# Kernel optimization log

Measured on AMD Instinct MI355X. Metric: run time of the kernel, lower is better.

The kernel has to match this reference:

```python
import jax, jax.numpy as jnp
import numpy as np

GROUP_SIZE = 128


def dequant_rtn(qweight, scale, zero_point):
    # qweight: [O, I] int, scale/zero_point: [O, I//GROUP_SIZE]
    O, I = qweight.shape
    G = scale.shape[1]
    gs = I // G
    q = qweight.reshape(O, G, gs).astype(jnp.float32)
    zp = zero_point.astype(jnp.float32)[:, :, None]
    w = (q - zp) * scale[:, :, None]
    return w.reshape(O, I)


def setup_inputs() -> dict:
    key = jax.random.key(0)
    k1, k2, k3, k4, k5 = jax.random.split(key, 5)
    B, S, I, O = 2, 2048, 4096, 11008
    G = I // GROUP_SIZE
    x = jax.random.normal(k1, (B, S, I), dtype=jnp.float32)
    qweight = jax.random.randint(k2, (O, I), 0, 16, dtype=jnp.int32)
    scale = jax.random.uniform(k3, (O, G), dtype=jnp.float32) * 0.02 + 1e-3
    zero_point = jax.random.randint(k4, (O, G), 0, 16, dtype=jnp.int32)
    bias = jax.random.normal(k5, (O,), dtype=jnp.float32)
    return {"x": x, "qweight": qweight, "scale": scale,
            "zero_point": zero_point, "bias": bias}


def reference(x, qweight, scale, zero_point, bias):
    # weight-only path: dequant weight, then F.linear(x, w, bias)
    w = dequant_rtn(qweight, scale, zero_point)  # [O, I] fp32
    return jnp.einsum('bsi,oi->bso', x, w) + bias
```

## Files before the change

### kernel.cpp

```cpp
#include <hip/hip_runtime.h>
#include <cstdint>
#include <cstddef>

typedef __attribute__((ext_vector_type(4))) int i32x4;
typedef __bf16 bf16;
typedef __attribute__((ext_vector_type(8))) __bf16 bf16x8;
typedef __attribute__((ext_vector_type(4))) float f32x4;

#define BM 128
#define BN 128
#define BKB 128
#define GROUP_M 16

__device__ __forceinline__ unsigned bf16_rne(float f) {
  unsigned u = __float_as_uint(f);
  unsigned r = 0x7FFFu + ((u >> 16) & 1u);
  return ((u + r) >> 16) & 0xFFFFu;
}
__device__ __forceinline__ unsigned pack2(float a, float b) {
  return bf16_rne(a) | (bf16_rne(b) << 16);
}
__device__ __forceinline__ int pack4i8(int a, int b, int c, int d) {
  return (a & 0xFF) | ((b & 0xFF) << 8) | ((c & 0xFF) << 16) | (d << 24);
}
__device__ __forceinline__ int q_i8(float v) {
  v = fminf(fmaxf(v, -127.0f), 127.0f);
  return __float2int_rn(v);
}

__global__ __launch_bounds__(256) void prep_kernel(
    const float* __restrict__ x, char* __restrict__ xq, float* __restrict__ xscale,
    int M,
    const int* __restrict__ q, const float* __restrict__ scale,
    const int* __restrict__ zp, char* __restrict__ wq, float* __restrict__ wscale,
    int K, int G) {
  __shared__ float red[4];
  const int b = blockIdx.x;
  const int tid = threadIdx.x;
  float f[16];

  if (b < M) {
    const float4* src = (const float4*)(x + (size_t)b * K);
#pragma unroll
    for (int i = 0; i < 4; ++i) {
      float4 v = src[tid + 256 * i];
      f[4 * i + 0] = v.x; f[4 * i + 1] = v.y;
      f[4 * i + 2] = v.z; f[4 * i + 3] = v.w;
    }
  } else {
    const int row = b - M;
    const int4* src = (const int4*)(q + (size_t)row * K);
    const float* srow = scale + (size_t)row * G;
    const int*   zrow = zp + (size_t)row * G;
#pragma unroll
    for (int i = 0; i < 4; ++i) {
      const int j = tid + 256 * i;
      const int g = j >> 5;
      const float s = srow[g];
      const float nzs = -s * (float)zrow[g];
      int4 qv = src[j];
      f[4 * i + 0] = fmaf((float)qv.x, s, nzs);
      f[4 * i + 1] = fmaf((float)qv.y, s, nzs);
      f[4 * i + 2] = fmaf((float)qv.z, s, nzs);
      f[4 * i + 3] = fmaf((float)qv.w, s, nzs);
    }
  }

  float m = 0.f;
#pragma unroll
  for (int j = 0; j < 16; ++j) m = fmaxf(m, fabsf(f[j]));
#pragma unroll
  for (int off = 32; off >= 1; off >>= 1) m = fmaxf(m, __shfl_xor(m, off));
  if ((tid & 63) == 0) red[tid >> 6] = m;
  __syncthreads();
  m = fmaxf(fmaxf(red[0], red[1]), fmaxf(red[2], red[3]));

  const float inv = m > 0.f ? 127.0f / m : 0.f;
  int pk[4];
#pragma unroll
  for (int i = 0; i < 4; ++i)
    pk[i] = pack4i8(q_i8(f[4 * i + 0] * inv), q_i8(f[4 * i + 1] * inv),
                    q_i8(f[4 * i + 2] * inv), q_i8(f[4 * i + 3] * inv));

  char* dst = (b < M) ? (xq + (size_t)b * K) : (wq + (size_t)(b - M) * K);
  int* dst_i32 = (int*)dst;
#pragma unroll
  for (int i = 0; i < 4; ++i) dst_i32[tid + 256 * i] = pk[i];

  if (tid == 0) {
    if (b < M) xscale[b] = m * (1.0f / 127.0f);
    else       wscale[b - M] = m * (1.0f / 127.0f);
  }
}

typedef __attribute__((address_space(1))) void gas_void;
typedef __attribute__((address_space(3))) void las_void;

__device__ __forceinline__ void load_lds16(const void* g, void* l) {
  __builtin_amdgcn_global_load_lds((gas_void*)g, (las_void*)l, 16, 0, 0);
}

__global__ __launch_bounds__(256) void gemm_i8_kernel(
    const char* __restrict__ A,
    const char* __restrict__ Bw,
    const float* __restrict__ ascale,
    const float* __restrict__ bscale,
    const float* __restrict__ bias,
    float* __restrict__ C,
    int M, int N, int K) {
  __shared__ __align__(16) char Alds[BM * BKB];
  __shared__ __align__(16) char Blds[BN * BKB];
  const int tid  = threadIdx.x;
  const int wave = tid >> 6;
  const int lane = tid & 63;
  const int quad = lane >> 4;
  const int l16  = lane & 15;

  const int nbm = M / BM;
  const int nbn = N / BN;
  int flat = blockIdx.x;
  int per_group = GROUP_M * nbn;
  int gid = flat / per_group;
  int rem = flat - gid * per_group;
  int gm = nbm - gid * GROUP_M;
  if (gm > GROUP_M) gm = GROUP_M;
  const int bm = (gid * GROUP_M + (rem % gm)) * BM;
  const int bn = (rem / gm) * BN;

  const int wm = (wave & 1) * 64;
  const int wn = (wave >> 1) * 64;

  i32x4 acc[4][4];
#pragma unroll
  for (int i = 0; i < 4; ++i)
#pragma unroll
    for (int j = 0; j < 4; ++j)
      acc[i][j] = (i32x4){0, 0, 0, 0};

  for (int kt = 0; kt < K; kt += BKB) {
#pragma unroll
    for (int t = 0; t < 4; ++t) {
      int s0 = (wave * 4 + t) * 64;
      int s  = s0 + lane;
      int m  = s >> 3;
      int kq = (s & 7) ^ (m & 7);
      load_lds16(A  + (size_t)(bm + m) * K + kt + kq * 16, &Alds[s0 * 16]);
      load_lds16(Bw + (size_t)(bn + m) * K + kt + kq * 16, &Blds[s0 * 16]);
    }
    __syncthreads();

#pragma unroll
    for (int ks = 0; ks < 2; ++ks) {
      i32x4 af[4], bfr[4];
#pragma unroll
      for (int tm = 0; tm < 4; ++tm) {
        int m  = wm + tm * 16 + l16;
        int kq = ks * 4 + quad;
        af[tm] = *(const i32x4*)&Alds[(m * 8 + (kq ^ (m & 7))) * 16];
      }
#pragma unroll
      for (int tn = 0; tn < 4; ++tn) {
        int n  = wn + tn * 16 + l16;
        int kq = ks * 4 + quad;
        bfr[tn] = *(const i32x4*)&Blds[(n * 8 + (kq ^ (n & 7))) * 16];
      }
#pragma unroll
      for (int tm = 0; tm < 4; ++tm)
#pragma unroll
        for (int tn = 0; tn < 4; ++tn)
          acc[tm][tn] = __builtin_amdgcn_mfma_i32_16x16x64_i8(
              af[tm], bfr[tn], acc[tm][tn], 0, 0, 0);
    }
    __syncthreads();
  }

#pragma unroll
  for (int tn = 0; tn < 4; ++tn) {
    int col = bn + wn + tn * 16 + l16;
    float bv = bias[col];
    float ws = bscale[col];
#pragma unroll
    for (int tm = 0; tm < 4; ++tm) {
      int row0 = bm + wm + tm * 16 + quad * 4;
#pragma unroll
      for (int v = 0; v < 4; ++v) {
        float val = ascale[row0 + v] * ws * (float)acc[tm][tn][v] + bv;
        __builtin_nontemporal_store(val, &C[(size_t)(row0 + v) * N + col]);
      }
    }
  }
}

__global__ __launch_bounds__(256) void gemm_fused_kernel(
    const float* __restrict__ X, const int* __restrict__ Q,
    const float* __restrict__ scale, const int* __restrict__ zp,
    const float* __restrict__ bias, float* __restrict__ C,
    int M, int N, int K, int G) {
  __shared__ __align__(16) bf16 Alds[128 * 64];
  __shared__ __align__(16) bf16 Blds[128 * 64];
  const int tid  = threadIdx.x;
  const int wave = tid >> 6;
  const int lane = tid & 63;
  const int quad = lane >> 4;
  const int l16  = lane & 15;
  const int bm = blockIdx.y * 128;
  const int bn = blockIdx.x * 128;
  const int wm = (wave & 1) * 64;
  const int wn = (wave >> 1) * 64;

  f32x4 acc[4][4];
#pragma unroll
  for (int i = 0; i < 4; ++i)
#pragma unroll
    for (int j = 0; j < 4; ++j)
      acc[i][j] = (f32x4){0.f, 0.f, 0.f, 0.f};

  for (int kt = 0; kt < K; kt += 64) {
#pragma unroll
    for (int i = 0; i < 4; ++i) {
      int c = tid + i * 256;
      int m = c >> 3;
      int kq = (c & 7) ^ (m & 7);
      const float* src = X + (size_t)(bm + m) * K + kt + kq * 8;
      float4 v0 = *(const float4*)src;
      float4 v1 = *(const float4*)(src + 4);
      uint4 p;
      p.x = pack2(v0.x, v0.y); p.y = pack2(v0.z, v0.w);
      p.z = pack2(v1.x, v1.y); p.w = pack2(v1.z, v1.w);
      *(uint4*)&Alds[c * 8] = p;
    }
#pragma unroll
    for (int i = 0; i < 4; ++i) {
      int c = tid + i * 256;
      int n = c >> 3;
      int kq = (c & 7) ^ (n & 7);
      int kcol = kt + kq * 8;
      size_t row = (size_t)(bn + n);
      int g = kcol >> 7;
      float s = scale[row * G + g];
      float z = (float)zp[row * G + g];
      const int* src = Q + row * K + kcol;
      int4 q0 = *(const int4*)src;
      int4 q1 = *(const int4*)(src + 4);
      uint4 p;
      p.x = pack2(((float)q0.x - z) * s, ((float)q0.y - z) * s);
      p.y = pack2(((float)q0.z - z) * s, ((float)q0.w - z) * s);
      p.z = pack2(((float)q1.x - z) * s, ((float)q1.y - z) * s);
      p.w = pack2(((float)q1.z - z) * s, ((float)q1.w - z) * s);
      *(uint4*)&Blds[c * 8] = p;
    }
    __syncthreads();

#pragma unroll
    for (int ks = 0; ks < 2; ++ks) {
      bf16x8 af[4], bfr[4];
#pragma unroll
      for (int tm = 0; tm < 4; ++tm) {
        int m  = wm + tm * 16 + l16;
        int kq = ks * 4 + quad;
        af[tm] = *(const bf16x8*)&Alds[(m * 8 + (kq ^ (m & 7))) * 8];
      }
#pragma unroll
      for (int tn = 0; tn < 4; ++tn) {
        int n  = wn + tn * 16 + l16;
        int kq = ks * 4 + quad;
        bfr[tn] = *(const bf16x8*)&Blds[(n * 8 + (kq ^ (n & 7))) * 8];
      }
#pragma unroll
      for (int tm = 0; tm < 4; ++tm)
#pragma unroll
        for (int tn = 0; tn < 4; ++tn)
          acc[tm][tn] = __builtin_amdgcn_mfma_f32_16x16x32_bf16(
              af[tm], bfr[tn], acc[tm][tn], 0, 0, 0);
    }
    __syncthreads();
  }

#pragma unroll
  for (int tn = 0; tn < 4; ++tn) {
    int col = bn + wn + tn * 16 + l16;
    float bv = bias[col];
#pragma unroll
    for (int tm = 0; tm < 4; ++tm) {
      int row0 = bm + wm + tm * 16 + quad * 4;
#pragma unroll
      for (int v = 0; v < 4; ++v)
        C[(size_t)(row0 + v) * N + col] = acc[tm][tn][v] + bv;
    }
  }
}

extern "C" void kernel_launch(void* const* d_in, const int* in_sizes, int n_in,
                              void* d_out, int out_size, void* d_ws, size_t ws_size,
                              hipStream_t stream) {
  const float* x     = (const float*)d_in[0];
  const int*   qw    = (const int*)d_in[1];
  const float* scale = (const float*)d_in[2];
  const int*   zp    = (const int*)d_in[3];
  const float* bias  = (const float*)d_in[4];
  float* out = (float*)d_out;

  const int O = in_sizes[4];
  const int I = (int)(in_sizes[1] / O);
  const int M = (int)(in_sizes[0] / I);
  const int G = in_sizes[2] / O;
  const int K = I, N = O;

  size_t off_xq = 0;
  size_t off_xs = off_xq + (size_t)M * K;
  size_t off_wq = (off_xs + (size_t)M * 4 + 255) & ~(size_t)255;
  size_t off_ws_ = off_wq + (size_t)N * K;
  size_t need   = ((off_ws_ + (size_t)N * 4 + 255) & ~(size_t)255);

  if (ws_size >= need && K == 4096) {
    char*  xq = (char*)d_ws + off_xq;
    float* xs = (float*)((char*)d_ws + off_xs);
    char*  wq = (char*)d_ws + off_wq;
    float* wsc = (float*)((char*)d_ws + off_ws_);

    prep_kernel<<<M + N, 256, 0, stream>>>(x, xq, xs, M, qw, scale, zp, wq, wsc, K, G);

    int nblocks = (M / BM) * (N / BN);
    gemm_i8_kernel<<<nblocks, 256, 0, stream>>>(xq, wq, xs, wsc, bias, out, M, N, K);
  } else {
    dim3 gemm_grid((unsigned)(N / 128), (unsigned)(M / 128));
    gemm_fused_kernel<<<gemm_grid, 256, 0, stream>>>(x, qw, scale, zp, bias, out,
                                                     M, N, K, G);
  }
}
```

Baseline: 579.2 us.

## Add 256x256 int8 GEMM kernel with XCD swizzle and phased double buffering

Adds a new int8 MFMA GEMM that uses 256x256 output tiles with 512 threads (8 waves), double-buffered LDS staging via global_load_lds, and an XCD-aware block remap plus grouped ordering. Each K-tile is split into four compute phases that interleave the next tile's global-to-LDS loads with MFMA work, and wave priority is raised around the MFMA bursts. The larger tile is meant to raise operand reuse and cut global and LDS traffic per FLOP compared with the 128x128 kernel. In exchange it needs 128KB of LDS and more accumulator registers, which limits occupancy to one block per CU. The old kernel is kept as a fallback when shapes do not divide evenly.

```diff
diff --git a/kernel.cpp b/kernel.cpp
--- a/kernel.cpp
+++ b/kernel.cpp
@@ -11,6 +11,8 @@
 #define BN 128
 #define BKB 128
 #define GROUP_M 16
+#define GM256 4
+#define NXCD 8
 
 __device__ __forceinline__ unsigned bf16_rne(float f) {
   unsigned u = __float_as_uint(f);
@@ -100,13 +102,154 @@
   __builtin_amdgcn_global_load_lds((gas_void*)g, (las_void*)l, 16, 0, 0);
 }
 
-__global__ __launch_bounds__(256) void gemm_i8_kernel(
+
+#define STAGE_A(buf, half, ktb) do {                                          \
+    load_lds16(A + abase + (size_t)(half) * 128 * K + (size_t)(ktb) + off0,   \
+               &Al[buf][(half) * 16384 + d0w]);                               \
+    load_lds16(A + abase + (size_t)(half) * 128 * K + (size_t)(ktb) + off1,   \
+               &Al[buf][(half) * 16384 + d1w]);                               \
+  } while (0)
+
+#define STAGE_B(buf, half, ktb) do {                                          \
+    load_lds16(Bw + bbase + (size_t)(half) * 128 * K + (size_t)(ktb) + off0,  \
+               &Bl[buf][(half) * 16384 + d0w]);                               \
+    load_lds16(Bw + bbase + (size_t)(half) * 128 * K + (size_t)(ktb) + off1,  \
+               &Bl[buf][(half) * 16384 + d1w]);                               \
+  } while (0)
+
+#define PHASE(CUR, MH, NH, STAGE_STMT, WAIT_STMT) do {                        \
+    i32x4 afr[4][2], bfr[2][2];                                               \
+    _Pragma("unroll")                                                         \
+    for (int tm = 0; tm < 4; ++tm) {                                          \
+      _Pragma("unroll")                                                       \
+      for (int ks = 0; ks < 2; ++ks) {                                        \
+        int row = wmb + (MH) * 64 + tm * 16 + l16;                            \
+        int kq  = ks * 4 + quad;                                              \
+        afr[tm][ks] =                                                         \
+            *(const i32x4*)&Al[CUR][(row * 8 + (kq ^ (row & 7))) * 16];       \
+      }                                                                       \
+    }                                                                         \
+    _Pragma("unroll")                                                         \
+    for (int tn = 0; tn < 2; ++tn) {                                          \
+      _Pragma("unroll")                                                       \
+      for (int ks = 0; ks < 2; ++ks) {                                        \
+        int row = wnb + (NH) * 32 + tn * 16 + l16;                            \
+        int kq  = ks * 4 + quad;                                              \
+        bfr[tn][ks] =                                                         \
+            *(const i32x4*)&Bl[CUR][(row * 8 + (kq ^ (row & 7))) * 16];       \
+      }                                                                       \
+    }                                                                         \
+    STAGE_STMT;                                                               \
+    __builtin_amdgcn_s_barrier();                                             \
+    asm volatile("s_waitcnt lgkmcnt(0)" ::: "memory");                        \
+    __builtin_amdgcn_sched_barrier(0);                                        \
+    __builtin_amdgcn_s_setprio(1);                                            \
+    _Pragma("unroll")                                                         \
+    for (int tm = 0; tm < 4; ++tm) {                                          \
+      _Pragma("unroll")                                                       \
+      for (int tn = 0; tn < 2; ++tn) {                                        \
+        _Pragma("unroll")                                                     \
+        for (int ks = 0; ks < 2; ++ks) {                                      \
+          acc[(MH) * 4 + tm][(NH) * 2 + tn] =                                 \
+              __builtin_amdgcn_mfma_i32_16x16x64_i8(                          \
+                  afr[tm][ks], bfr[tn][ks],                                   \
+                  acc[(MH) * 4 + tm][(NH) * 2 + tn], 0, 0, 0);                \
+        }                                                                     \
+      }                                                                       \
+    }                                                                         \
+    __builtin_amdgcn_s_setprio(0);                                            \
+    WAIT_STMT;                                                                \
+    __builtin_amdgcn_s_barrier();                                             \
+    __builtin_amdgcn_sched_barrier(0);                                        \
+  } while (0)
+
+__global__ __launch_bounds__(512) void gemm_i8_256(
     const char* __restrict__ A,
     const char* __restrict__ Bw,
     const float* __restrict__ ascale,
     const float* __restrict__ bscale,
     const float* __restrict__ bias,
     float* __restrict__ C,
+    int M, int N, int K) {
+  __shared__ __align__(16) char Al[2][256 * 128];
+  __shared__ __align__(16) char Bl[2][256 * 128];
+  const int tid  = threadIdx.x;
+  const int wave = tid >> 6;
+  const int lane = tid & 63;
+  const int quad = lane >> 4;
+  const int l16  = lane & 15;
+  const int wmb  = (wave >> 2) * 128;
+  const int wnb  = (wave & 3) * 64;
+
+  const int nbm = M / 256, nbn = N / 256;
+  const int cpx = (nbm * nbn) / NXCD;
+  const int swz = ((int)blockIdx.x % NXCD) * cpx + (int)blockIdx.x / NXCD;
+  const int per_group = GM256 * nbn;
+  const int gid = swz / per_group;
+  const int rem = swz - gid * per_group;
+  int gm = nbm - gid * GM256; if (gm > GM256) gm = GM256;
+  const int bm = (gid * GM256 + (rem % gm)) * 256;
+  const int bn = (rem / gm) * 256;
+
+  const int sA = tid, sB = 512 + tid;
+  const int m0 = sA >> 3, m1 = sB >> 3;
+  const size_t off0 = (size_t)m0 * K + (size_t)(((sA & 7) ^ (m0 & 7)) * 16);
+  const size_t off1 = (size_t)m1 * K + (size_t)(((sB & 7) ^ (m1 & 7)) * 16);
+  const int d0w = (0 * 512 + wave * 64) * 16;
+  const int d1w = (1 * 512 + wave * 64) * 16;
+  const size_t abase = (size_t)bm * K;
+  const size_t bbase = (size_t)bn * K;
+  const int NT = K / 128;
+
+  i32x4 acc[8][4];
+#pragma unroll
+  for (int i = 0; i < 8; ++i)
+#pragma unroll
+    for (int j = 0; j < 4; ++j)
+      acc[i][j] = (i32x4){0, 0, 0, 0};
+
+  STAGE_A(0, 0, 0);
+  STAGE_A(0, 1, 0);
+  STAGE_B(0, 0, 0);
+  STAGE_B(0, 1, 0);
+  asm volatile("s_waitcnt vmcnt(0)" ::: "memory");
+  __builtin_amdgcn_s_barrier();
+  __builtin_amdgcn_sched_barrier(0);
+
+  for (int t = 0; t < NT; ++t) {
+    const int cur = t & 1;
+    const int nxt = cur ^ 1;
+    const int kt1 = (t + 1) * 128;
+    const bool s1 = (t + 1) < NT;
+
+    PHASE(cur, 0, 0, { if (s1) { STAGE_A(nxt, 0, kt1); STAGE_A(nxt, 1, kt1); } }, {});
+    PHASE(cur, 1, 0, { if (s1) { STAGE_B(nxt, 0, kt1); STAGE_B(nxt, 1, kt1); } }, {});
+    PHASE(cur, 0, 1, {}, {});
+    PHASE(cur, 1, 1, {},
+          { asm volatile("s_waitcnt vmcnt(0)" ::: "memory"); });
+  }
+
+#pragma unroll
+  for (int tn = 0; tn < 4; ++tn) {
+    int col = bn + wnb + tn * 16 + l16;
+    float bv = bias[col];
+    float ws = bscale[col];
+#pragma unroll
+    for (int tm = 0; tm < 8; ++tm) {
+      int row0 = bm + wmb + tm * 16 + quad * 4;
+#pragma unroll
+      for (int v = 0; v < 4; ++v) {
+        float val = ascale[row0 + v] * ws * (float)acc[tm][tn][v] + bv;
+        __builtin_nontemporal_store(val, &C[(size_t)(row0 + v) * N + col]);
+      }
+    }
+  }
+}
+
+__global__ __launch_bounds__(256) void gemm_i8_kernel(
+    const char* __restrict__ A, const char* __restrict__ Bw,
+    const float* __restrict__ ascale, const float* __restrict__ bscale,
+    const float* __restrict__ bias, float* __restrict__ C,
     int M, int N, int K) {
   __shared__ __align__(16) char Alds[BM * BKB];
   __shared__ __align__(16) char Blds[BN * BKB];
@@ -320,8 +463,13 @@
 
     prep_kernel<<<M + N, 256, 0, stream>>>(x, xq, xs, M, qw, scale, zp, wq, wsc, K, G);
 
-    int nblocks = (M / BM) * (N / BN);
-    gemm_i8_kernel<<<nblocks, 256, 0, stream>>>(xq, wq, xs, wsc, bias, out, M, N, K);
+    const int nb256 = (M / 256) * (N / 256);
+    if ((M % 256) == 0 && (N % 256) == 0 && (nb256 % NXCD) == 0) {
+      gemm_i8_256<<<nb256, 512, 0, stream>>>(xq, wq, xs, wsc, bias, out, M, N, K);
+    } else {
+      int nblocks = (M / BM) * (N / BN);
+      gemm_i8_kernel<<<nblocks, 256, 0, stream>>>(xq, wq, xs, wsc, bias, out, M, N, K);
+    }
   } else {
     dim3 gemm_grid((unsigned)(N / 128), (unsigned)(M / 128));
     gemm_fused_kernel<<<gemm_grid, 256, 0, stream>>>(x, qw, scale, zp, bias, out,
```

Result: faster. 557.5 us (-3.8%).
